# Optimization experiments

Hardware: AMD Instinct MI355X
Metric: run time of the kernel (lower is better)

The kernel has to match this reference:

```python
import jax, jax.numpy as jnp
import numpy as np

VOCAB, POS_V, NER_V, DEPREL_V = 50000, 50, 10, 40
EMB, POS_D, NER_D, MEM = 300, 30, 30, 200
NUM_LAYERS = 2


def setup_inputs() -> dict:
    key = jax.random.key(0)
    ks = jax.random.split(key, 12)
    B, L = 32, 100
    adj = jax.random.randint(ks[0], (B, L, L), 0, DEPREL_V)
    words = jax.random.randint(ks[1], (B, L), 0, VOCAB)
    pos = jax.random.randint(ks[2], (B, L), 0, POS_V)
    ner = jax.random.randint(ks[3], (B, L), 0, NER_V)
    s = 0.02
    emb = jax.random.normal(ks[4], (VOCAB, EMB), jnp.float32) * s
    pos_emb = jax.random.normal(ks[5], (POS_V, POS_D), jnp.float32) * s
    ner_emb = jax.random.normal(ks[6], (NER_V, NER_D), jnp.float32) * s
    deprel_emb = jax.random.normal(ks[7], (DEPREL_V, MEM), jnp.float32) * s
    deprel_emb = deprel_emb.at[0].set(0.0)  # padding_idx=0
    in_dim = EMB + POS_D + NER_D
    Wp = jax.random.normal(ks[8], (MEM, in_dim), jnp.float32) * s
    bp = jnp.zeros((MEM,), jnp.float32)
    W0 = jax.random.normal(ks[9], (MEM, MEM), jnp.float32) * s
    b0 = jnp.zeros((MEM,), jnp.float32)
    W1 = jax.random.normal(ks[10], (MEM, MEM), jnp.float32) * s
    b1 = jnp.zeros((MEM,), jnp.float32)
    return {"adj": adj, "words": words, "pos": pos, "ner": ner,
            "emb": emb, "pos_emb": pos_emb, "ner_emb": ner_emb,
            "deprel_emb": deprel_emb, "Wp": Wp, "bp": bp,
            "W0": W0, "b0": b0, "W1": W1, "b1": b1}


def reference(adj, words, pos, ner, emb, pos_emb, ner_emb, deprel_emb,
              Wp, bp, W0, b0, W1, b1):
    # embedding lookups + concat  -> [B, L, in_dim]
    embs = jnp.concatenate([emb[words], pos_emb[pos], ner_emb[ner]], axis=-1)
    # preprocessor linear (diagonal_deprel branch)  -> [B, L, D]
    x = embs @ Wp.T + bp
    # per-edge relation embedding gather  -> [B, L, L, D]
    deprel_adj = deprel_emb[adj]
    adj_m = (adj != 0).astype(jnp.float32)            # [B, L, L]
    denom = adj_m.sum(2)[..., None] + 1.0             # [B, L, 1]
    mask = ((adj_m.sum(2) + adj_m.sum(1)) == 0)[..., None]  # [B, L, 1]
    for W, b in ((W0, b0), (W1, b1)):
        # diagonal deprel aggregation: (deprel_adj * x[:,None]) summed over neighbors
        Ax = jnp.einsum('blmd,bmd->bld', deprel_adj, x)
        AxW = (Ax @ W.T + b) + (x @ W.T + b)
        x = jax.nn.relu(AxW / denom)
    return x, mask
```

## Files before the change

kernel.cpp:

```cpp
#include <hip/hip_runtime.h>
#include <hip/hip_bf16.h>

#define BB 32
#define LL 100
#define DD 200
#define KIN 360
#define NP (BB*LL)
#define RNUM 40
#define LT 13
#define NT 8

__device__ __forceinline__ void fma4(float4& a, const float4& w, float s) {
    a.x = fmaf(w.x, s, a.x);
    a.y = fmaf(w.y, s, a.y);
    a.z = fmaf(w.z, s, a.z);
    a.w = fmaf(w.w, s, a.w);
}
__device__ __forceinline__ unsigned bf16rn(float f) {
    unsigned u = __float_as_uint(f);
    return (u + 0x7fffu + ((u >> 16) & 1u)) >> 16;
}
__device__ __forceinline__ unsigned pk2(float a, float b) {
    return bf16rn(a) | (bf16rn(b) << 16);
}
__device__ __forceinline__ float lo16(unsigned u) { return __uint_as_float(u << 16); }
__device__ __forceinline__ float hi16(unsigned u) { return __uint_as_float(u & 0xffff0000u); }

__global__ __launch_bounds__(256) void prep_transpose_kernel(
        const int* __restrict__ adj,
        const float* __restrict__ Wp, const float* __restrict__ W0, const float* __restrict__ W1,
        float* __restrict__ WpT, float* __restrict__ W0T, float* __restrict__ W1T,
        float* __restrict__ invd, float* __restrict__ mask_out) {
    int bid = blockIdx.x, tid = threadIdx.x;
    if (bid < 25) {
        int t = bid * 256 + tid;
        int half = t & 1;
        int pl = t >> 1;
        int b = pl / LL, l = pl % LL;
        const int4* row = (const int4*)(adj + (size_t)pl * LL);
        int q0 = half ? 13 : 0, q1 = half ? 25 : 13;
        int rc = 0;
        for (int i = q0; i < q1; ++i) {
            int4 a = row[i];
            rc += (a.x != 0) + (a.y != 0) + (a.z != 0) + (a.w != 0);
        }
        const int* base = adj + (size_t)b * LL * LL + l;
        int cc = 0;
        for (int m = half * 50; m < half * 50 + 50; ++m) cc += (base[(size_t)m * LL] != 0);
        rc += __shfl_xor(rc, 1);
        cc += __shfl_xor(cc, 1);
        if (!half) {
            invd[pl] = 1.0f / (float)(rc + 1);
            mask_out[pl] = (rc + cc == 0) ? 1.0f : 0.0f;
        }
    } else {
        int i = (bid - 25) * 256 + tid;
        if (i < 18000) {
            int k = i / 50, o = (i % 50) * 4;
            float4 v;
            v.x = Wp[(size_t)(o + 0) * KIN + k];
            v.y = Wp[(size_t)(o + 1) * KIN + k];
            v.z = Wp[(size_t)(o + 2) * KIN + k];
            v.w = Wp[(size_t)(o + 3) * KIN + k];
            ((float4*)WpT)[i] = v;
        } else if (i < 28000) {
            int q = i - 18000;
            int k = q / 50, o = (q % 50) * 4;
            float4 v;
            v.x = W0[(size_t)(o + 0) * DD + k];
            v.y = W0[(size_t)(o + 1) * DD + k];
            v.z = W0[(size_t)(o + 2) * DD + k];
            v.w = W0[(size_t)(o + 3) * DD + k];
            ((float4*)W0T)[q] = v;
        } else if (i < 38000) {
            int q = i - 28000;
            int k = q / 50, o = (q % 50) * 4;
            float4 v;
            v.x = W1[(size_t)(o + 0) * DD + k];
            v.y = W1[(size_t)(o + 1) * DD + k];
            v.z = W1[(size_t)(o + 2) * DD + k];
            v.w = W1[(size_t)(o + 3) * DD + k];
            ((float4*)W1T)[q] = v;
        }
    }
}

__global__ __launch_bounds__(256) void embed_gemv_kernel(
        const int* __restrict__ words, const int* __restrict__ pos, const int* __restrict__ ner,
        const float* __restrict__ emb, const float* __restrict__ pose, const float* __restrict__ nere,
        const float* __restrict__ wpt, const float* __restrict__ bp,
        float* __restrict__ xA) {
    __shared__ float es[8 * KIN];
    __shared__ float4 red[4 * 8 * 50];
    int tid = threadIdx.x;
    int pbase = blockIdx.x * 8;

    const float2* emb2  = (const float2*)emb;
    const float2* pose2 = (const float2*)pose;
    const float2* nere2 = (const float2*)nere;
    float2* es2 = (float2*)es;
    for (int idx = tid; idx < 8 * 180; idx += 256) {
        int p = idx / 180, j2 = idx % 180;
        int gp = pbase + p;
        float2 v;
        if (j2 < 150)      v = emb2[(size_t)words[gp] * 150 + j2];
        else if (j2 < 165) v = pose2[pos[gp] * 15 + (j2 - 150)];
        else               v = nere2[ner[gp] * 15 + (j2 - 165)];
        es2[idx] = v;
    }
    __syncthreads();

    int lane = tid & 63, w = tid >> 6;
    bool act = lane < 50;
    int oq = act ? lane : 49;
    int kq0 = w * 24;
    int kqn = (w < 3) ? 24 : 18;
    const float4* wt4 = (const float4*)wpt;
    const float4* es4 = (const float4*)es;

    float4 a[8];
    #pragma unroll
    for (int p = 0; p < 8; ++p) a[p] = make_float4(0.f, 0.f, 0.f, 0.f);

    for (int k = 0; k < kqn; ++k) {
        int kq = kq0 + k;
        float4 w0 = wt4[(size_t)(4 * kq + 0) * 50 + oq];
        float4 w1 = wt4[(size_t)(4 * kq + 1) * 50 + oq];
        float4 w2 = wt4[(size_t)(4 * kq + 2) * 50 + oq];
        float4 w3 = wt4[(size_t)(4 * kq + 3) * 50 + oq];
        #pragma unroll
        for (int p = 0; p < 8; ++p) {
            float4 s = es4[p * 90 + kq];
            fma4(a[p], w0, s.x); fma4(a[p], w1, s.y);
            fma4(a[p], w2, s.z); fma4(a[p], w3, s.w);
        }
    }
    if (act) {
        #pragma unroll
        for (int p = 0; p < 8; ++p) red[w * 400 + p * 50 + oq] = a[p];
    }
    __syncthreads();
    for (int t = tid; t < 400; t += 256) {
        int oq2 = t % 50;
        float4 v0 = red[t], v1 = red[400 + t], v2 = red[800 + t], v3 = red[1200 + t];
        float4 bb = ((const float4*)bp)[oq2];
        float4 v;
        v.x = v0.x + v1.x + v2.x + v3.x + bb.x;
        v.y = v0.y + v1.y + v2.y + v3.y + bb.y;
        v.z = v0.z + v1.z + v2.z + v3.z + bb.z;
        v.w = v0.w + v1.w + v2.w + v3.w + bb.w;
        ((float4*)xA)[(size_t)(pbase + t / 50) * 50 + oq2] = v;
    }
}

__global__ __launch_bounds__(512) void layer_kernel(
        const float* __restrict__ x, const int* __restrict__ adj,
        const float* __restrict__ deprel, const float* __restrict__ wt,
        const float* __restrict__ bias, const float* __restrict__ invd,
        float* __restrict__ out) {
    __shared__ uint2 deps_b[RNUM * 50];
    __shared__ unsigned adjp[LT * 25];
    __shared__ float4 Sh[2 * 650];
    __shared__ float4 Sfin[650];
    int b = blockIdx.y, tile = blockIdx.x;
    int l0 = tile * LT;
    int lcnt = min(LT, LL - l0);
    int tid = threadIdx.x;
    const float4* x4 = (const float4*)x;

    for (int i = tid; i < RNUM * 50; i += 512) {
        float4 v = ((const float4*)deprel)[i];
        deps_b[i] = make_uint2(pk2(v.x, v.y), pk2(v.z, v.w));
    }
    for (int i = tid; i < lcnt * 25; i += 512) {
        int li = i / 25, mg = i % 25;
        int4 a = ((const int4*)(adj + (size_t)(b * LL + l0 + li) * LL))[mg];
        adjp[i] = (unsigned)a.x | ((unsigned)a.y << 8) | ((unsigned)a.z << 16) | ((unsigned)a.w << 24);
    }
    __syncthreads();

    int lane = tid & 63, w = tid >> 6;
    int lg = w & 3, mh = w >> 2;
    bool act = lane < 50;
    int dq = lane;

    float4 acc[4];
    #pragma unroll
    for (int i = 0; i < 4; ++i) acc[i] = make_float4(0.f, 0.f, 0.f, 0.f);
    if (act) {
        int mg0 = mh ? 13 : 0, mg1 = mh ? 25 : 13;
        for (int mg = mg0; mg < mg1; ++mg) {
            unsigned ap[4];
            #pragma unroll
            for (int i = 0; i < 4; ++i) {
                int li = lg + 4 * i;
                ap[i] = (li < lcnt) ? adjp[li * 25 + mg] : 0u;
            }
            #pragma unroll
            for (int mm = 0; mm < 4; ++mm) {
                float4 xv = x4[(size_t)(b * LL + 4 * mg + mm) * 50 + dq];
                #pragma unroll
                for (int i = 0; i < 4; ++i) {
                    unsigned r = (ap[i] >> (8 * mm)) & 0xffu;
                    uint2 dv = deps_b[r * 50 + dq];
                    acc[i].x = fmaf(lo16(dv.x), xv.x, acc[i].x);
                    acc[i].y = fmaf(hi16(dv.x), xv.y, acc[i].y);
                    acc[i].z = fmaf(lo16(dv.y), xv.z, acc[i].z);
                    acc[i].w = fmaf(hi16(dv.y), xv.w, acc[i].w);
                }
            }
        }
        #pragma unroll
        for (int i = 0; i < 4; ++i) {
            int li = lg + 4 * i;
            if (li < lcnt) Sh[mh * 650 + li * 50 + dq] = acc[i];
        }
    }
    __syncthreads();

    for (int t = tid; t < 650; t += 512) {
        int li = t / 50;
        if (li < lcnt) {
            float4 s0 = Sh[t], s1 = Sh[650 + t];
            float4 xr = x4[(size_t)(b * LL + l0 + li) * 50 + (t % 50)];
            float4 s;
            s.x = s0.x + s1.x + xr.x; s.y = s0.y + s1.y + xr.y;
            s.z = s0.z + s1.z + xr.z; s.w = s0.w + s1.w + xr.w;
            Sfin[t] = s;
        }
    }
    __syncthreads();

    const float4* wt4 = (const float4*)wt;
    int oq = act ? lane : 49;
    float4 ba[4];
    #pragma unroll
    for (int i = 0; i < 4; ++i) ba[i] = make_float4(0.f, 0.f, 0.f, 0.f);
    for (int k = 0; k < 25; ++k) {
        int kq = mh * 25 + k;
        float4 w0 = wt4[(size_t)(4 * kq + 0) * 50 + oq];
        float4 w1 = wt4[(size_t)(4 * kq + 1) * 50 + oq];
        float4 w2 = wt4[(size_t)(4 * kq + 2) * 50 + oq];
        float4 w3 = wt4[(size_t)(4 * kq + 3) * 50 + oq];
        #pragma unroll
        for (int i = 0; i < 4; ++i) {
            int li = lg + 4 * i;
            int lic = li < lcnt ? li : lcnt - 1;
            float4 s = Sfin[lic * 50 + kq];
            fma4(ba[i], w0, s.x); fma4(ba[i], w1, s.y);
            fma4(ba[i], w2, s.z); fma4(ba[i], w3, s.w);
        }
    }
    if (act) {
        #pragma unroll
        for (int i = 0; i < 4; ++i) {
            int li = lg + 4 * i;
            if (li < lcnt) Sh[mh * 650 + li * 50 + oq] = ba[i];
        }
    }
    __syncthreads();

    for (int t = tid; t < 650; t += 512) {
        int li = t / 50, oq2 = t % 50;
        if (li < lcnt) {
            float4 v0 = Sh[t], v1 = Sh[650 + t];
            float4 bb = ((const float4*)bias)[oq2];
            int p = b * LL + l0 + li;
            float sc = invd[p];
            float4 v;
            v.x = fmaxf((v0.x + v1.x + 2.f * bb.x) * sc, 0.f);
            v.y = fmaxf((v0.y + v1.y + 2.f * bb.y) * sc, 0.f);
            v.z = fmaxf((v0.z + v1.z + 2.f * bb.z) * sc, 0.f);
            v.w = fmaxf((v0.w + v1.w + 2.f * bb.w) * sc, 0.f);
            ((float4*)out)[(size_t)p * 50 + oq2] = v;
        }
    }
}

extern "C" void kernel_launch(void* const* d_in, const int* in_sizes, int n_in,
                              void* d_out, int out_size, void* d_ws, size_t ws_size,
                              hipStream_t stream) {
    const int*   adj   = (const int*)d_in[0];
    const int*   words = (const int*)d_in[1];
    const int*   pos   = (const int*)d_in[2];
    const int*   ner   = (const int*)d_in[3];
    const float* emb   = (const float*)d_in[4];
    const float* pose  = (const float*)d_in[5];
    const float* nere  = (const float*)d_in[6];
    const float* dep   = (const float*)d_in[7];
    const float* Wp    = (const float*)d_in[8];
    const float* bp    = (const float*)d_in[9];
    const float* W0    = (const float*)d_in[10];
    const float* b0    = (const float*)d_in[11];
    const float* W1    = (const float*)d_in[12];
    const float* b1    = (const float*)d_in[13];
    float* out = (float*)d_out;
    float* ws  = (float*)d_ws;

    float* xA   = ws;
    float* xB   = ws + 640000;
    float* WpT  = ws + 1280000;
    float* W0T  = ws + 1352000;
    float* W1T  = ws + 1392000;
    float* invd = ws + 1432000;

    prep_transpose_kernel<<<25 + 149, 256, 0, stream>>>(adj, Wp, W0, W1, WpT, W0T, W1T,
                                                        invd, out + (size_t)NP * DD);
    embed_gemv_kernel<<<NP / 8, 256, 0, stream>>>(words, pos, ner, emb, pose, nere,
                                                  WpT, bp, xA);
    layer_kernel<<<dim3(NT, BB), 512, 0, stream>>>(xA, adj, dep, W0T, b0, invd, xB);
    layer_kernel<<<dim3(NT, BB), 512, 0, stream>>>(xB, adj, dep, W1T, b1, invd, out);
}
```

Before: 75.72 us.

## Fuse all stages into one persistent kernel with software grid barriers

Replaces the four separate launches (prep/transpose, embedding GEMV, two layer kernels) with a single persistent kernel of 256 blocks that synchronizes stages through an atomic-counter grid barrier. Adjacency packing and bf16 deprel conversion move into the prep stage and are stored globally, so the layer stages reuse the packed tiles across both layers instead of rebuilding them. The embedding GEMV now processes 16 positions per block across 512 threads. This aims to remove launch gaps and per-kernel setup. In exchange it adds a memset plus barrier spin overhead, and it relies on all 256 blocks being co-resident or the barrier deadlocks.

```diff
diff --git a/kernel.cpp b/kernel.cpp
--- a/kernel.cpp
+++ b/kernel.cpp
@@ -5,10 +5,21 @@
 #define LL 100
 #define DD 200
 #define KIN 360
-#define NP (BB*LL)
+#define NP 3200
 #define RNUM 40
 #define LT 13
-#define NT 8
+#define NBLK 256
+#define NTHR 512
+
+#define OFF_XA    0
+#define OFF_XB    640000
+#define OFF_WPT   1280000
+#define OFF_W0T   1352000
+#define OFF_W1T   1392000
+#define OFF_INVD  1432000
+#define OFF_DEPP  1435200
+#define OFF_ADJP  1439200
+#define OFF_BAR   1519200
 
 __device__ __forceinline__ void fma4(float4& a, const float4& w, float s) {
     a.x = fmaf(w.x, s, a.x);
@@ -26,254 +37,295 @@
 __device__ __forceinline__ float lo16(unsigned u) { return __uint_as_float(u << 16); }
 __device__ __forceinline__ float hi16(unsigned u) { return __uint_as_float(u & 0xffff0000u); }
 
-__global__ __launch_bounds__(256) void prep_transpose_kernel(
-        const int* __restrict__ adj,
-        const float* __restrict__ Wp, const float* __restrict__ W0, const float* __restrict__ W1,
-        float* __restrict__ WpT, float* __restrict__ W0T, float* __restrict__ W1T,
-        float* __restrict__ invd, float* __restrict__ mask_out) {
+__device__ __forceinline__ void grid_barrier(unsigned* bar) {
+    __syncthreads();
+    if (threadIdx.x == 0) {
+        __threadfence();
+        unsigned g = __hip_atomic_load(bar + 1, __ATOMIC_ACQUIRE, __HIP_MEMORY_SCOPE_AGENT);
+        unsigned a = __hip_atomic_fetch_add(bar, 1u, __ATOMIC_ACQ_REL, __HIP_MEMORY_SCOPE_AGENT);
+        if (a == NBLK - 1) {
+            __hip_atomic_store(bar, 0u, __ATOMIC_RELEASE, __HIP_MEMORY_SCOPE_AGENT);
+            __hip_atomic_fetch_add(bar + 1, 1u, __ATOMIC_RELEASE, __HIP_MEMORY_SCOPE_AGENT);
+        } else {
+            while (__hip_atomic_load(bar + 1, __ATOMIC_ACQUIRE, __HIP_MEMORY_SCOPE_AGENT) == g)
+                __builtin_amdgcn_s_sleep(1);
+        }
+        __threadfence();
+    }
+    __syncthreads();
+}
+
+__global__ __launch_bounds__(NTHR, 4) void fused_kernel(
+        const int* __restrict__ adj, const int* __restrict__ words,
+        const int* __restrict__ pos, const int* __restrict__ ner,
+        const float* __restrict__ emb, const float* __restrict__ pose,
+        const float* __restrict__ nere, const float* __restrict__ dep,
+        const float* __restrict__ Wp, const float* __restrict__ bp,
+        const float* __restrict__ W0, const float* __restrict__ b0,
+        const float* __restrict__ W1, const float* __restrict__ b1,
+        float* ws, float* out) {
+    __shared__ alignas(16) char smem[48768];
+    unsigned* bar = (unsigned*)(ws + OFF_BAR);
+    float* xA = ws + OFF_XA;
+    float* xB = ws + OFF_XB;
+    float* wpT = ws + OFF_WPT;
+    float* w0T = ws + OFF_W0T;
+    float* w1T = ws + OFF_W1T;
+    float* invd_g = ws + OFF_INVD;
+    uint2* depp_g = (uint2*)(ws + OFF_DEPP);
+    unsigned* adjp_g = (unsigned*)(ws + OFF_ADJP);
+
     int bid = blockIdx.x, tid = threadIdx.x;
-    if (bid < 25) {
-        int t = bid * 256 + tid;
-        int half = t & 1;
-        int pl = t >> 1;
-        int b = pl / LL, l = pl % LL;
-        const int4* row = (const int4*)(adj + (size_t)pl * LL);
-        int q0 = half ? 13 : 0, q1 = half ? 25 : 13;
-        int rc = 0;
-        for (int i = q0; i < q1; ++i) {
-            int4 a = row[i];
-            rc += (a.x != 0) + (a.y != 0) + (a.z != 0) + (a.w != 0);
-        }
-        const int* base = adj + (size_t)b * LL * LL + l;
-        int cc = 0;
-        for (int m = half * 50; m < half * 50 + 50; ++m) cc += (base[(size_t)m * LL] != 0);
-        rc += __shfl_xor(rc, 1);
-        cc += __shfl_xor(cc, 1);
-        if (!half) {
-            invd[pl] = 1.0f / (float)(rc + 1);
-            mask_out[pl] = (rc + cc == 0) ? 1.0f : 0.0f;
-        }
-    } else {
-        int i = (bid - 25) * 256 + tid;
-        if (i < 18000) {
-            int k = i / 50, o = (i % 50) * 4;
+
+    {
+        int t = bid * NTHR + tid;
+        if (t < 18000) {
+            int k = t / 50, o = (t % 50) * 4;
             float4 v;
             v.x = Wp[(size_t)(o + 0) * KIN + k];
             v.y = Wp[(size_t)(o + 1) * KIN + k];
             v.z = Wp[(size_t)(o + 2) * KIN + k];
             v.w = Wp[(size_t)(o + 3) * KIN + k];
-            ((float4*)WpT)[i] = v;
-        } else if (i < 28000) {
-            int q = i - 18000;
+            ((float4*)wpT)[t] = v;
+        } else if (t < 28000) {
+            int q = t - 18000;
             int k = q / 50, o = (q % 50) * 4;
             float4 v;
             v.x = W0[(size_t)(o + 0) * DD + k];
             v.y = W0[(size_t)(o + 1) * DD + k];
             v.z = W0[(size_t)(o + 2) * DD + k];
             v.w = W0[(size_t)(o + 3) * DD + k];
-            ((float4*)W0T)[q] = v;
-        } else if (i < 38000) {
-            int q = i - 28000;
+            ((float4*)w0T)[q] = v;
+        } else if (t < 38000) {
+            int q = t - 28000;
             int k = q / 50, o = (q % 50) * 4;
             float4 v;
             v.x = W1[(size_t)(o + 0) * DD + k];
             v.y = W1[(size_t)(o + 1) * DD + k];
             v.z = W1[(size_t)(o + 2) * DD + k];
             v.w = W1[(size_t)(o + 3) * DD + k];
-            ((float4*)W1T)[q] = v;
+            ((float4*)w1T)[q] = v;
+        } else if (t < 44400) {
+            int item = t - 38000;
+            int half = item & 1, pl = item >> 1;
+            int b = pl / LL, l = pl % LL;
+            const int4* row = (const int4*)(adj + (size_t)pl * LL);
+            int q0 = half ? 13 : 0, q1 = half ? 25 : 13;
+            int rc = 0;
+            for (int i = q0; i < q1; ++i) {
+                int4 a = row[i];
+                rc += (a.x != 0) + (a.y != 0) + (a.z != 0) + (a.w != 0);
+            }
+            const int* base = adj + (size_t)b * LL * LL + l;
+            int cc = 0;
+            for (int m = half * 50; m < half * 50 + 50; ++m) cc += (base[(size_t)m * LL] != 0);
+            rc += __shfl_xor(rc, 1);
+            cc += __shfl_xor(cc, 1);
+            if (!half) {
+                invd_g[pl] = 1.0f / (float)(rc + 1);
+                out[(size_t)NP * DD + pl] = (rc + cc == 0) ? 1.0f : 0.0f;
+            }
+        } else if (t < 46400) {
+            int i = t - 44400;
+            float4 v = ((const float4*)dep)[i];
+            depp_g[i] = make_uint2(pk2(v.x, v.y), pk2(v.z, v.w));
+        } else if (t < 126400) {
+            int i = t - 46400;
+            int4 a = ((const int4*)adj)[i];
+            adjp_g[i] = (unsigned)a.x | ((unsigned)a.y << 8) |
+                        ((unsigned)a.z << 16) | ((unsigned)a.w << 24);
         }
     }
-}
-
-__global__ __launch_bounds__(256) void embed_gemv_kernel(
-        const int* __restrict__ words, const int* __restrict__ pos, const int* __restrict__ ner,
-        const float* __restrict__ emb, const float* __restrict__ pose, const float* __restrict__ nere,
-        const float* __restrict__ wpt, const float* __restrict__ bp,
-        float* __restrict__ xA) {
-    __shared__ float es[8 * KIN];
-    __shared__ float4 red[4 * 8 * 50];
-    int tid = threadIdx.x;
-    int pbase = blockIdx.x * 8;
-
-    const float2* emb2  = (const float2*)emb;
-    const float2* pose2 = (const float2*)pose;
-    const float2* nere2 = (const float2*)nere;
-    float2* es2 = (float2*)es;
-    for (int idx = tid; idx < 8 * 180; idx += 256) {
-        int p = idx / 180, j2 = idx % 180;
-        int gp = pbase + p;
-        float2 v;
-        if (j2 < 150)      v = emb2[(size_t)words[gp] * 150 + j2];
-        else if (j2 < 165) v = pose2[pos[gp] * 15 + (j2 - 150)];
-        else               v = nere2[ner[gp] * 15 + (j2 - 165)];
-        es2[idx] = v;
+
+    grid_barrier(bar);
+
+    if (bid < 200) {
+        float* es = (float*)smem;
+        float4* red = (float4*)(smem + 23040);
+        int pbase = bid * 16;
+        float2* es2 = (float2*)es;
+        for (int idx = tid; idx < 16 * 180; idx += NTHR) {
+            int p = idx / 180, j2 = idx % 180;
+            int gp = pbase + p;
+            float2 v;
+            if (j2 < 150)      v = ((const float2*)emb)[(size_t)words[gp] * 150 + j2];
+            else if (j2 < 165) v = ((const float2*)pose)[pos[gp] * 15 + (j2 - 150)];
+            else               v = ((const float2*)nere)[ner[gp] * 15 + (j2 - 165)];
+            es2[idx] = v;
+        }
+        __syncthreads();
+
+        int lane = tid & 63, wv = tid >> 6;
+        int c = wv >> 2, w4 = wv & 3;
+        bool act = lane < 50;
+        int oq = act ? lane : 49;
+        int kq0 = w4 * 24;
+        int kqn = (w4 < 3) ? 24 : 18;
+        const float4* wt4 = (const float4*)wpT;
+        const float4* es4 = (const float4*)es;
+        float4 a[8];
+        #pragma unroll
+        for (int p = 0; p < 8; ++p) a[p] = make_float4(0.f, 0.f, 0.f, 0.f);
+        for (int k = 0; k < kqn; ++k) {
+            int kq = kq0 + k;
+            float4 w0 = wt4[(size_t)(4 * kq + 0) * 50 + oq];
+            float4 w1 = wt4[(size_t)(4 * kq + 1) * 50 + oq];
+            float4 w2 = wt4[(size_t)(4 * kq + 2) * 50 + oq];
+            float4 w3 = wt4[(size_t)(4 * kq + 3) * 50 + oq];
+            #pragma unroll
+            for (int p = 0; p < 8; ++p) {
+                float4 s = es4[(c * 8 + p) * 90 + kq];
+                fma4(a[p], w0, s.x); fma4(a[p], w1, s.y);
+                fma4(a[p], w2, s.z); fma4(a[p], w3, s.w);
+            }
+        }
+        float4* redc = red + c * 800;
+        if (w4 >= 2 && act) {
+            #pragma unroll
+            for (int p = 0; p < 8; ++p) redc[(w4 - 2) * 400 + p * 50 + oq] = a[p];
+        }
+        __syncthreads();
+        if (w4 < 2 && act) {
+            #pragma unroll
+            for (int p = 0; p < 8; ++p) {
+                float4 r = redc[w4 * 400 + p * 50 + oq];
+                r.x += a[p].x; r.y += a[p].y; r.z += a[p].z; r.w += a[p].w;
+                redc[w4 * 400 + p * 50 + oq] = r;
+            }
+        }
+        __syncthreads();
+        for (int t2 = tid; t2 < 800; t2 += NTHR) {
+            int pp = t2 / 50, oq2 = t2 % 50;
+            float4* rc2 = red + (pp >> 3) * 800;
+            float4 v0 = rc2[(pp & 7) * 50 + oq2];
+            float4 v1 = rc2[400 + (pp & 7) * 50 + oq2];
+            float4 bb = ((const float4*)bp)[oq2];
+            float4 v;
+            v.x = v0.x + v1.x + bb.x; v.y = v0.y + v1.y + bb.y;
+            v.z = v0.z + v1.z + bb.z; v.w = v0.w + v1.w + bb.w;
+            ((float4*)xA)[(size_t)(pbase + pp) * 50 + oq2] = v;
+        }
     }
-    __syncthreads();
-
-    int lane = tid & 63, w = tid >> 6;
-    bool act = lane < 50;
-    int oq = act ? lane : 49;
-    int kq0 = w * 24;
-    int kqn = (w < 3) ? 24 : 18;
-    const float4* wt4 = (const float4*)wpt;
-    const float4* es4 = (const float4*)es;
-
-    float4 a[8];
-    #pragma unroll
-    for (int p = 0; p < 8; ++p) a[p] = make_float4(0.f, 0.f, 0.f, 0.f);
-
-    for (int k = 0; k < kqn; ++k) {
-        int kq = kq0 + k;
-        float4 w0 = wt4[(size_t)(4 * kq + 0) * 50 + oq];
-        float4 w1 = wt4[(size_t)(4 * kq + 1) * 50 + oq];
-        float4 w2 = wt4[(size_t)(4 * kq + 2) * 50 + oq];
-        float4 w3 = wt4[(size_t)(4 * kq + 3) * 50 + oq];
-        #pragma unroll
-        for (int p = 0; p < 8; ++p) {
-            float4 s = es4[p * 90 + kq];
-            fma4(a[p], w0, s.x); fma4(a[p], w1, s.y);
-            fma4(a[p], w2, s.z); fma4(a[p], w3, s.w);
-        }
-    }
-    if (act) {
-        #pragma unroll
-        for (int p = 0; p < 8; ++p) red[w * 400 + p * 50 + oq] = a[p];
-    }
-    __syncthreads();
-    for (int t = tid; t < 400; t += 256) {
-        int oq2 = t % 50;
-        float4 v0 = red[t], v1 = red[400 + t], v2 = red[800 + t], v3 = red[1200 + t];
-        float4 bb = ((const float4*)bp)[oq2];
-        float4 v;
-        v.x = v0.x + v1.x + v2.x + v3.x + bb.x;
-        v.y = v0.y + v1.y + v2.y + v3.y + bb.y;
-        v.z = v0.z + v1.z + v2.z + v3.z + bb.z;
-        v.w = v0.w + v1.w + v2.w + v3.w + bb.w;
-        ((float4*)xA)[(size_t)(pbase + t / 50) * 50 + oq2] = v;
-    }
-}
-
-__global__ __launch_bounds__(512) void layer_kernel(
-        const float* __restrict__ x, const int* __restrict__ adj,
-        const float* __restrict__ deprel, const float* __restrict__ wt,
-        const float* __restrict__ bias, const float* __restrict__ invd,
-        float* __restrict__ out) {
-    __shared__ uint2 deps_b[RNUM * 50];
-    __shared__ unsigned adjp[LT * 25];
-    __shared__ float4 Sh[2 * 650];
-    __shared__ float4 Sfin[650];
-    int b = blockIdx.y, tile = blockIdx.x;
+
+    uint2* deps_b = (uint2*)smem;
+    unsigned* adjp = (unsigned*)(smem + 16000);
+    float4* Sh = (float4*)(smem + 17312);
+    float4* Sfin = (float4*)(smem + 38112);
+    int b = bid >> 3, tile = bid & 7;
     int l0 = tile * LT;
     int lcnt = min(LT, LL - l0);
-    int tid = threadIdx.x;
-    const float4* x4 = (const float4*)x;
-
-    for (int i = tid; i < RNUM * 50; i += 512) {
-        float4 v = ((const float4*)deprel)[i];
-        deps_b[i] = make_uint2(pk2(v.x, v.y), pk2(v.z, v.w));
-    }
-    for (int i = tid; i < lcnt * 25; i += 512) {
-        int li = i / 25, mg = i % 25;
-        int4 a = ((const int4*)(adj + (size_t)(b * LL + l0 + li) * LL))[mg];
-        adjp[i] = (unsigned)a.x | ((unsigned)a.y << 8) | ((unsigned)a.z << 16) | ((unsigned)a.w << 24);
-    }
-    __syncthreads();
-
-    int lane = tid & 63, w = tid >> 6;
-    int lg = w & 3, mh = w >> 2;
+    int lane = tid & 63, wv = tid >> 6;
+    int lg = wv & 3, mh = wv >> 2;
     bool act = lane < 50;
     int dq = lane;
 
-    float4 acc[4];
-    #pragma unroll
-    for (int i = 0; i < 4; ++i) acc[i] = make_float4(0.f, 0.f, 0.f, 0.f);
-    if (act) {
-        int mg0 = mh ? 13 : 0, mg1 = mh ? 25 : 13;
-        for (int mg = mg0; mg < mg1; ++mg) {
-            unsigned ap[4];
+    for (int layer = 0; layer < 2; ++layer) {
+        grid_barrier(bar);
+        const float* xin = layer ? xB : xA;
+        float* xout = layer ? out : xB;
+        const float* wt = layer ? w1T : w0T;
+        const float* bias = layer ? b1 : b0;
+        const float4* x4 = (const float4*)xin;
+
+        if (layer == 0) {
+            for (int i = tid; i < 2000; i += NTHR) deps_b[i] = depp_g[i];
+            for (int i = tid; i < lcnt * 25; i += NTHR)
+                adjp[i] = adjp_g[(b * LL + l0) * 25 + i];
+        }
+        __syncthreads();
+
+        float4 acc[4];
+        #pragma unroll
+        for (int i = 0; i < 4; ++i) acc[i] = make_float4(0.f, 0.f, 0.f, 0.f);
+        if (act) {
+            int mg0 = mh ? 13 : 0, mg1 = mh ? 25 : 13;
+            for (int mg = mg0; mg < mg1; ++mg) {
+                unsigned ap[4];
+                #pragma unroll
+                for (int i = 0; i < 4; ++i) {
+                    int li = lg + 4 * i;
+                    ap[i] = (li < lcnt) ? adjp[li * 25 + mg] : 0u;
+                }
+                #pragma unroll
+                for (int mm = 0; mm < 4; ++mm) {
+                    float4 xv = x4[(size_t)(b * LL + 4 * mg + mm) * 50 + dq];
+                    #pragma unroll
+                    for (int i = 0; i < 4; ++i) {
+                        unsigned r = (ap[i] >> (8 * mm)) & 0xffu;
+                        uint2 dv = deps_b[r * 50 + dq];
+                        acc[i].x = fmaf(lo16(dv.x), xv.x, acc[i].x);
+                        acc[i].y = fmaf(hi16(dv.x), xv.y, acc[i].y);
+                        acc[i].z = fmaf(lo16(dv.y), xv.z, acc[i].z);
+                        acc[i].w = fmaf(hi16(dv.y), xv.w, acc[i].w);
+                    }
+                }
+            }
             #pragma unroll
             for (int i = 0; i < 4; ++i) {
                 int li = lg + 4 * i;
-                ap[i] = (li < lcnt) ? adjp[li * 25 + mg] : 0u;
-            }
-            #pragma unroll
-            for (int mm = 0; mm < 4; ++mm) {
-                float4 xv = x4[(size_t)(b * LL + 4 * mg + mm) * 50 + dq];
-                #pragma unroll
-                for (int i = 0; i < 4; ++i) {
-                    unsigned r = (ap[i] >> (8 * mm)) & 0xffu;
-                    uint2 dv = deps_b[r * 50 + dq];
-                    acc[i].x = fmaf(lo16(dv.x), xv.x, acc[i].x);
-                    acc[i].y = fmaf(hi16(dv.x), xv.y, acc[i].y);
-                    acc[i].z = fmaf(lo16(dv.y), xv.z, acc[i].z);
-                    acc[i].w = fmaf(hi16(dv.y), xv.w, acc[i].w);
-                }
-            }
-        }
+                if (li < lcnt) Sh[mh * 650 + li * 50 + dq] = acc[i];
+            }
+        }
+        __syncthreads();
+
+        for (int t2 = tid; t2 < 650; t2 += NTHR) {
+            int li = t2 / 50;
+            if (li < lcnt) {
+                float4 s0 = Sh[t2], s1 = Sh[650 + t2];
+                float4 xr = x4[(size_t)(b * LL + l0 + li) * 50 + (t2 % 50)];
+                float4 s;
+                s.x = s0.x + s1.x + xr.x; s.y = s0.y + s1.y + xr.y;
+                s.z = s0.z + s1.z + xr.z; s.w = s0.w + s1.w + xr.w;
+                Sfin[t2] = s;
+            }
+        }
+        __syncthreads();
+
+        const float4* wt4 = (const float4*)wt;
+        int oq = act ? lane : 49;
+        float4 ba[4];
         #pragma unroll
-        for (int i = 0; i < 4; ++i) {
-            int li = lg + 4 * i;
-            if (li < lcnt) Sh[mh * 650 + li * 50 + dq] = acc[i];
-        }
-    }
-    __syncthreads();
-
-    for (int t = tid; t < 650; t += 512) {
-        int li = t / 50;
-        if (li < lcnt) {
-            float4 s0 = Sh[t], s1 = Sh[650 + t];
-            float4 xr = x4[(size_t)(b * LL + l0 + li) * 50 + (t % 50)];
-            float4 s;
-            s.x = s0.x + s1.x + xr.x; s.y = s0.y + s1.y + xr.y;
-            s.z = s0.z + s1.z + xr.z; s.w = s0.w + s1.w + xr.w;
-            Sfin[t] = s;
-        }
-    }
-    __syncthreads();
-
-    const float4* wt4 = (const float4*)wt;
-    int oq = act ? lane : 49;
-    float4 ba[4];
-    #pragma unroll
-    for (int i = 0; i < 4; ++i) ba[i] = make_float4(0.f, 0.f, 0.f, 0.f);
-    for (int k = 0; k < 25; ++k) {
-        int kq = mh * 25 + k;
-        float4 w0 = wt4[(size_t)(4 * kq + 0) * 50 + oq];
-        float4 w1 = wt4[(size_t)(4 * kq + 1) * 50 + oq];
-        float4 w2 = wt4[(size_t)(4 * kq + 2) * 50 + oq];
-        float4 w3 = wt4[(size_t)(4 * kq + 3) * 50 + oq];
-        #pragma unroll
-        for (int i = 0; i < 4; ++i) {
-            int li = lg + 4 * i;
-            int lic = li < lcnt ? li : lcnt - 1;
-            float4 s = Sfin[lic * 50 + kq];
-            fma4(ba[i], w0, s.x); fma4(ba[i], w1, s.y);
-            fma4(ba[i], w2, s.z); fma4(ba[i], w3, s.w);
-        }
-    }
-    if (act) {
-        #pragma unroll
-        for (int i = 0; i < 4; ++i) {
-            int li = lg + 4 * i;
-            if (li < lcnt) Sh[mh * 650 + li * 50 + oq] = ba[i];
-        }
-    }
-    __syncthreads();
-
-    for (int t = tid; t < 650; t += 512) {
-        int li = t / 50, oq2 = t % 50;
-        if (li < lcnt) {
-            float4 v0 = Sh[t], v1 = Sh[650 + t];
-            float4 bb = ((const float4*)bias)[oq2];
-            int p = b * LL + l0 + li;
-            float sc = invd[p];
-            float4 v;
-            v.x = fmaxf((v0.x + v1.x + 2.f * bb.x) * sc, 0.f);
-            v.y = fmaxf((v0.y + v1.y + 2.f * bb.y) * sc, 0.f);
-            v.z = fmaxf((v0.z + v1.z + 2.f * bb.z) * sc, 0.f);
-            v.w = fmaxf((v0.w + v1.w + 2.f * bb.w) * sc, 0.f);
-            ((float4*)out)[(size_t)p * 50 + oq2] = v;
-        }
+        for (int i = 0; i < 4; ++i) ba[i] = make_float4(0.f, 0.f, 0.f, 0.f);
+        for (int k = 0; k < 25; ++k) {
+            int kq = mh * 25 + k;
+            float4 w0 = wt4[(size_t)(4 * kq + 0) * 50 + oq];
+            float4 w1 = wt4[(size_t)(4 * kq + 1) * 50 + oq];
+            float4 w2 = wt4[(size_t)(4 * kq + 2) * 50 + oq];
+            float4 w3 = wt4[(size_t)(4 * kq + 3) * 50 + oq];
+            #pragma unroll
+            for (int i = 0; i < 4; ++i) {
+                int li = lg + 4 * i;
+                int lic = li < lcnt ? li : lcnt - 1;
+                float4 s = Sfin[lic * 50 + kq];
+                fma4(ba[i], w0, s.x); fma4(ba[i], w1, s.y);
+                fma4(ba[i], w2, s.z); fma4(ba[i], w3, s.w);
+            }
+        }
+        if (act) {
+            #pragma unroll
+            for (int i = 0; i < 4; ++i) {
+                int li = lg + 4 * i;
+                if (li < lcnt) Sh[mh * 650 + li * 50 + oq] = ba[i];
+            }
+        }
+        __syncthreads();
+
+        for (int t2 = tid; t2 < 650; t2 += NTHR) {
+            int li = t2 / 50, oq2 = t2 % 50;
+            if (li < lcnt) {
+                float4 v0 = Sh[t2], v1 = Sh[650 + t2];
+                float4 bb = ((const float4*)bias)[oq2];
+                int p = b * LL + l0 + li;
+                float sc = invd_g[p];
+                float4 v;
+                v.x = fmaxf((v0.x + v1.x + 2.f * bb.x) * sc, 0.f);
+                v.y = fmaxf((v0.y + v1.y + 2.f * bb.y) * sc, 0.f);
+                v.z = fmaxf((v0.z + v1.z + 2.f * bb.z) * sc, 0.f);
+                v.w = fmaxf((v0.w + v1.w + 2.f * bb.w) * sc, 0.f);
+                ((float4*)xout)[(size_t)p * 50 + oq2] = v;
+            }
+        }
+        __syncthreads();
     }
 }
 
@@ -297,17 +349,7 @@
     float* out = (float*)d_out;
     float* ws  = (float*)d_ws;
 
-    float* xA   = ws;
-    float* xB   = ws + 640000;
-    float* WpT  = ws + 1280000;
-    float* W0T  = ws + 1352000;
-    float* W1T  = ws + 1392000;
-    float* invd = ws + 1432000;
-
-    prep_transpose_kernel<<<25 + 149, 256, 0, stream>>>(adj, Wp, W0, W1, WpT, W0T, W1T,
-                                                        invd, out + (size_t)NP * DD);
-    embed_gemv_kernel<<<NP / 8, 256, 0, stream>>>(words, pos, ner, emb, pose, nere,
-                                                  WpT, bp, xA);
-    layer_kernel<<<dim3(NT, BB), 512, 0, stream>>>(xA, adj, dep, W0T, b0, invd, xB);
-    layer_kernel<<<dim3(NT, BB), 512, 0, stream>>>(xB, adj, dep, W1T, b1, invd, out);
-}
+    hipMemsetAsync(ws + OFF_BAR, 0, 8, stream);
+    fused_kernel<<<NBLK, NTHR, 0, stream>>>(adj, words, pos, ner, emb, pose, nere,
+                                            dep, Wp, bp, W0, b0, W1, b1, ws, out);
+}
```

Measured after the change: 256.7 us. +239.0%, slower.
